# Optimization experiments

Measured on AMD Instinct MI355X. Metric: run time of the kernel, lower is better.

## Reference

```python
import jax, jax.numpy as jnp
import numpy as np

LAYERS = [256, 512, 512, 256]
DIM = 20
BATCH = 131072
PERIOD = 0.1
AMP = 1.0


def tri(x):
    # triangle wave centered around 0 with period PERIOD, amplitude AMP
    # matches: amplitude/period * (period - abs(x % (2p) - p) - p/2)
    return AMP / PERIOD * (PERIOD - jnp.abs(jnp.mod(x, 2.0 * PERIOD) - PERIOD) - PERIOD / 2.0)


def cdist(a, b):
    # pairwise euclidean distance between rows of a [m,d] and b [n,d] -> [m,n]
    d2 = (jnp.sum(a * a, axis=1)[:, None]
          + jnp.sum(b * b, axis=1)[None, :]
          - 2.0 * (a @ b.T))
    return jnp.sqrt(jnp.maximum(d2, 0.0))


def setup_inputs() -> dict:
    key = jax.random.key(0)
    ks = jax.random.split(key, 1 + len(LAYERS) + len(LAYERS))
    inp = {"x": jax.random.normal(ks[0], (BATCH, LAYERS[0]), dtype=jnp.float32)}
    # layer_params: uniform in [-1, 1), shape [l, DIM]
    for i, l in enumerate(LAYERS):
        inp[f"p{i}"] = jax.random.uniform(ks[1 + i], (l, DIM), dtype=jnp.float32,
                                          minval=-1.0, maxval=1.0)
    # layer_biases: uniform in [-0.1, 0.1), shape [l, 1]; only indices 1..n-1 are used
    for i in (1, 2, 3):
        inp[f"b{i}"] = jax.random.uniform(ks[1 + len(LAYERS) + i], (LAYERS[i], 1),
                                          dtype=jnp.float32, minval=-1.0, maxval=1.0) * 0.1
    return inp


def reference(x, p0, p1, p2, p3, b1, b2, b3):
    params = [p0, p1, p2, p3]
    biases = [None, b1, b2, b3]
    n = len(params)
    z = x
    for i in range(n - 1):
        l, lnext = params[i], params[i + 1]
        # synthesized weight: [l_i, l_{i+1}]
        W = tri(cdist(l, lnext)) / np.sqrt(l.shape[0]).astype(np.float32)
        z = z @ W + biases[i + 1].T  # bias [l_{i+1},1].T broadcasts over batch
        if i < n - 2:
            z = jax.nn.relu(z)
    return z
```

## Files before the change

### kernel.cpp

```cpp
#include <hip/hip_runtime.h>
#include <hip/hip_fp16.h>

typedef _Float16 f16x8 __attribute__((ext_vector_type(8)));
typedef _Float16 f16x4 __attribute__((ext_vector_type(4)));
typedef float    f32x4 __attribute__((ext_vector_type(4)));

#define BATCH 131072

__global__ void synth_weights_kernel(const float* __restrict__ p0, const float* __restrict__ p1,
                                     const float* __restrict__ p2, const float* __restrict__ p3,
                                     _Float16* __restrict__ wt0, _Float16* __restrict__ wt1,
                                     _Float16* __restrict__ wt2)
{
    int idx = blockIdx.x * blockDim.x + threadIdx.x;
    const float* A; const float* B; _Float16* Wt; float scl; int e, k, n;
    if (idx < 131072)      { A = p0; B = p1; Wt = wt0; scl = 0.0625f;              e = idx;          k = e & 255; n = e >> 8; }
    else if (idx < 393216) { A = p1; B = p2; Wt = wt1; scl = 0.04419417382415922f; e = idx - 131072; k = e & 511; n = e >> 9; }
    else                   { A = p2; B = p3; Wt = wt2; scl = 0.04419417382415922f; e = idx - 393216; k = e & 511; n = e >> 9; }
    float d2 = 0.f;
#pragma unroll
    for (int t = 0; t < 20; ++t) {
        float df = A[k * 20 + t] - B[n * 20 + t];
        d2 += df * df;
    }
    float d  = sqrtf(d2);
    float md = fmodf(d, 0.2f);
    float w  = 10.0f * (0.05f - fabsf(md - 0.1f)) * scl;
    Wt[(size_t)e] = (_Float16)w;
}

__device__ __forceinline__ f16x8 ld_act(const char* act, int mi, int rl, int hi, int w)
{
    const int row = mi * 16 + rl;
    const int c   = w * 4 + hi;
    return *(const f16x8*)(act + row * 1024 + ((c ^ (row & 7)) << 4));
}

template<int K, int NI, int MI>
__device__ __forceinline__ void mm_reg(const char* act, const _Float16* __restrict__ Wt,
                                       int wc, int lane, int wid, f32x4 (&acc)[NI][MI])
{
    constexpr int NW = K / 32;
    const int rl = lane & 15;
    const int hi = lane >> 4;
    const int ph = (wid * (NW / 8)) & (NW - 1);

    const _Float16* wp[NI];
#pragma unroll
    for (int ni = 0; ni < NI; ++ni)
        wp[ni] = Wt + (size_t)(wc + ni * 16 + rl) * K + hi * 8;

    f16x8 wfA[NI], wfB[NI];
#pragma unroll
    for (int ni = 0; ni < NI; ++ni) wfA[ni] = *(const f16x8*)(wp[ni] + ph * 32);

#pragma unroll 1
    for (int w0 = 0; w0 < NW; w0 += 2) {
        const int wA = (w0 + ph) & (NW - 1);
        const int wB = (w0 + 1 + ph) & (NW - 1);
#pragma unroll
        for (int ni = 0; ni < NI; ++ni) wfB[ni] = *(const f16x8*)(wp[ni] + wB * 32);
        {
            f16x8 xf[MI];
#pragma unroll
            for (int mi = 0; mi < MI; ++mi) xf[mi] = ld_act(act, mi, rl, hi, wA);
            __builtin_amdgcn_s_setprio(1);
#pragma unroll
            for (int ni = 0; ni < NI; ++ni)
#pragma unroll
                for (int mi = 0; mi < MI; ++mi)
                    acc[ni][mi] = __builtin_amdgcn_mfma_f32_16x16x32_f16(wfA[ni], xf[mi], acc[ni][mi], 0, 0, 0);
            __builtin_amdgcn_s_setprio(0);
        }
        if (w0 + 2 < NW) {
            const int wC = (w0 + 2 + ph) & (NW - 1);
#pragma unroll
            for (int ni = 0; ni < NI; ++ni) wfA[ni] = *(const f16x8*)(wp[ni] + wC * 32);
        }
        {
            f16x8 xf[MI];
#pragma unroll
            for (int mi = 0; mi < MI; ++mi) xf[mi] = ld_act(act, mi, rl, hi, wB);
            __builtin_amdgcn_s_setprio(1);
#pragma unroll
            for (int ni = 0; ni < NI; ++ni)
#pragma unroll
                for (int mi = 0; mi < MI; ++mi)
                    acc[ni][mi] = __builtin_amdgcn_mfma_f32_16x16x32_f16(wfB[ni], xf[mi], acc[ni][mi], 0, 0, 0);
            __builtin_amdgcn_s_setprio(0);
        }
    }
}

template<int NI, int MI>
__device__ __forceinline__ void store_z(char* act, const float* __restrict__ bias,
                                        int wc, int lane, f32x4 (&acc)[NI][MI])
{
    const int rl = lane & 15;
    const int hi = lane >> 4;
#pragma unroll
    for (int ni = 0; ni < NI; ++ni) {
        const int n0 = wc + ni * 16 + hi * 4;
        const float4 bv = *(const float4*)(bias + n0);
#pragma unroll
        for (int mi = 0; mi < MI; ++mi) {
            const int m = mi * 16 + rl;
            f16x4 h;
            h[0] = (_Float16)fmaxf(acc[ni][mi][0] + bv.x, 0.0f);
            h[1] = (_Float16)fmaxf(acc[ni][mi][1] + bv.y, 0.0f);
            h[2] = (_Float16)fmaxf(acc[ni][mi][2] + bv.z, 0.0f);
            h[3] = (_Float16)fmaxf(acc[ni][mi][3] + bv.w, 0.0f);
            *(f16x4*)(act + m * 1024 + (((n0 >> 3) ^ (m & 7)) << 4) + (n0 & 7) * 2) = h;
        }
    }
}

__global__ __launch_bounds__(512, 2)
void fused_mlp_kernel(const float* __restrict__ x,
                      const _Float16* __restrict__ wt0, const _Float16* __restrict__ wt1,
                      const _Float16* __restrict__ wt2,
                      const float* __restrict__ b1, const float* __restrict__ b2,
                      const float* __restrict__ b3,
                      float* __restrict__ out)
{
    extern __shared__ char act[];
    const int tid  = threadIdx.x;
    const int lane = tid & 63;
    const int wid  = tid >> 6;
    const size_t m0 = (size_t)blockIdx.x * 128;

#pragma unroll
    for (int it = 0; it < 8; ++it) {
        const int c   = it * 512 + tid;
        const int row = c >> 5;
        const int c8  = c & 31;
        const float* src = x + (m0 + row) * 256 + c8 * 8;
        const float4 v0 = *(const float4*)src;
        const float4 v1 = *(const float4*)(src + 4);
        f16x8 h;
        h[0] = (_Float16)v0.x; h[1] = (_Float16)v0.y; h[2] = (_Float16)v0.z; h[3] = (_Float16)v0.w;
        h[4] = (_Float16)v1.x; h[5] = (_Float16)v1.y; h[6] = (_Float16)v1.z; h[7] = (_Float16)v1.w;
        *(f16x8*)(act + row * 1024 + ((c8 ^ (row & 7)) << 4)) = h;
    }
    __syncthreads();

    const int wc = wid * 64;

    {
        f32x4 acc[4][8] = {};
        mm_reg<256, 4, 8>(act, wt0, wc, lane, wid, acc);
        __syncthreads();
        store_z<4, 8>(act, b1, wc, lane, acc);
        __syncthreads();
    }

    {
        f32x4 acc[4][8] = {};
        mm_reg<512, 4, 8>(act, wt1, wc, lane, wid, acc);
        __syncthreads();
        store_z<4, 8>(act, b2, wc, lane, acc);
        __syncthreads();
    }

    {
        const int wc3 = wid * 32;
        f32x4 acc[2][8] = {};
        mm_reg<512, 2, 8>(act, wt2, wc3, lane, wid, acc);

        const int rl = lane & 15;
        const int hi = lane >> 4;
#pragma unroll
        for (int ni = 0; ni < 2; ++ni) {
            const int n0 = wc3 + ni * 16 + hi * 4;
            const float4 bv = *(const float4*)(b3 + n0);
#pragma unroll
            for (int mi = 0; mi < 8; ++mi) {
                const size_t m = m0 + mi * 16 + rl;
                f32x4 o;
                o[0] = acc[ni][mi][0] + bv.x;
                o[1] = acc[ni][mi][1] + bv.y;
                o[2] = acc[ni][mi][2] + bv.z;
                o[3] = acc[ni][mi][3] + bv.w;
                *(f32x4*)(out + m * 256 + n0) = o;
            }
        }
    }
}

extern "C" void kernel_launch(void* const* d_in, const int* in_sizes, int n_in,
                              void* d_out, int out_size, void* d_ws, size_t ws_size,
                              hipStream_t stream)
{
    const float* x  = (const float*)d_in[0];
    const float* p0 = (const float*)d_in[1];
    const float* p1 = (const float*)d_in[2];
    const float* p2 = (const float*)d_in[3];
    const float* p3 = (const float*)d_in[4];
    const float* b1 = (const float*)d_in[5];
    const float* b2 = (const float*)d_in[6];
    const float* b3 = (const float*)d_in[7];

    char* ws = (char*)d_ws;
    _Float16* wt0 = (_Float16*)(ws);
    _Float16* wt1 = (_Float16*)(ws + 262144);
    _Float16* wt2 = (_Float16*)(ws + 262144 + 524288);

    synth_weights_kernel<<<2048, 256, 0, stream>>>(p0, p1, p2, p3, wt0, wt1, wt2);

    fused_mlp_kernel<<<BATCH / 128, 512, 131072, stream>>>(x, wt0, wt1, wt2, b1, b2, b3,
                                                           (float*)d_out);
}
```

Measured before the change: 186.8 us.

## Pre-swizzle synthesized weights into per-lane fragment-order blobs for coalesced loads

The weight synthesis kernel now writes each weight matrix in the exact order the MFMA fragments are consumed: per wave, per k-step, per n-tile, with each lane's 8 halves contiguous. The MLP kernel then loads a fragment with a single contiguous 1 KB access per wave instead of strided row reads across K. This is meant to cut the number of global/L2 transactions for weight streaming. The MFMA loop order is also swapped to iterate ni inside mi.

```diff
diff --git a/kernel.cpp b/kernel.cpp
--- a/kernel.cpp
+++ b/kernel.cpp
@@ -9,14 +9,30 @@
 
 __global__ void synth_weights_kernel(const float* __restrict__ p0, const float* __restrict__ p1,
                                      const float* __restrict__ p2, const float* __restrict__ p3,
-                                     _Float16* __restrict__ wt0, _Float16* __restrict__ wt1,
-                                     _Float16* __restrict__ wt2)
-{
-    int idx = blockIdx.x * blockDim.x + threadIdx.x;
-    const float* A; const float* B; _Float16* Wt; float scl; int e, k, n;
-    if (idx < 131072)      { A = p0; B = p1; Wt = wt0; scl = 0.0625f;              e = idx;          k = e & 255; n = e >> 8; }
-    else if (idx < 393216) { A = p1; B = p2; Wt = wt1; scl = 0.04419417382415922f; e = idx - 131072; k = e & 511; n = e >> 9; }
-    else                   { A = p2; B = p3; Wt = wt2; scl = 0.04419417382415922f; e = idx - 393216; k = e & 511; n = e >> 9; }
+                                     _Float16* __restrict__ blob0, _Float16* __restrict__ blob1,
+                                     _Float16* __restrict__ blob2)
+{
+    const int idx = blockIdx.x * blockDim.x + threadIdx.x;
+    const float* A; const float* B; _Float16* Wt; float scl; int e, n, k;
+    if (idx < 131072) {
+        A = p0; B = p1; Wt = blob0; scl = 0.0625f; e = idx;
+        const int j = e & 7, lane = (e >> 3) & 63, t = e >> 9;
+        const int ni = t & 3, pw = t >> 2, w = pw & 7, wid = pw >> 3;
+        n = wid * 64 + ni * 16 + (lane & 15);
+        k = w * 32 + ((lane >> 4) << 3) + j;
+    } else if (idx < 393216) {
+        A = p1; B = p2; Wt = blob1; scl = 0.04419417382415922f; e = idx - 131072;
+        const int j = e & 7, lane = (e >> 3) & 63, t = e >> 9;
+        const int ni = t & 3, pw = t >> 2, w = pw & 15, wid = pw >> 4;
+        n = wid * 64 + ni * 16 + (lane & 15);
+        k = w * 32 + ((lane >> 4) << 3) + j;
+    } else {
+        A = p2; B = p3; Wt = blob2; scl = 0.04419417382415922f; e = idx - 393216;
+        const int j = e & 7, lane = (e >> 3) & 63, t = e >> 9;
+        const int ni = t & 1, pw = t >> 1, w = pw & 15, wid = pw >> 4;
+        n = wid * 32 + ni * 16 + (lane & 15);
+        k = w * 32 + ((lane >> 4) << 3) + j;
+    }
     float d2 = 0.f;
 #pragma unroll
     for (int t = 0; t < 20; ++t) {
@@ -36,46 +52,45 @@
     return *(const f16x8*)(act + row * 1024 + ((c ^ (row & 7)) << 4));
 }
 
-template<int K, int NI, int MI>
-__device__ __forceinline__ void mm_reg(const char* act, const _Float16* __restrict__ Wt,
-                                       int wc, int lane, int wid, f32x4 (&acc)[NI][MI])
-{
-    constexpr int NW = K / 32;
+template<int NW, int NI, int MI>
+__device__ __forceinline__ void mm_reg(const char* act, const _Float16* __restrict__ blob,
+                                       int lane, int wid, f32x4 (&acc)[NI][MI])
+{
     const int rl = lane & 15;
     const int hi = lane >> 4;
     const int ph = (wid * (NW / 8)) & (NW - 1);
 
-    const _Float16* wp[NI];
+    const char* wbase = (const char*)blob + ((size_t)wid * NW * NI) * 1024 + lane * 16;
+
+    f16x8 wfA[NI], wfB[NI];
 #pragma unroll
     for (int ni = 0; ni < NI; ++ni)
-        wp[ni] = Wt + (size_t)(wc + ni * 16 + rl) * K + hi * 8;
-
-    f16x8 wfA[NI], wfB[NI];
-#pragma unroll
-    for (int ni = 0; ni < NI; ++ni) wfA[ni] = *(const f16x8*)(wp[ni] + ph * 32);
+        wfA[ni] = *(const f16x8*)(wbase + (ph * NI + ni) * 1024);
 
 #pragma unroll 1
     for (int w0 = 0; w0 < NW; w0 += 2) {
         const int wA = (w0 + ph) & (NW - 1);
         const int wB = (w0 + 1 + ph) & (NW - 1);
 #pragma unroll
-        for (int ni = 0; ni < NI; ++ni) wfB[ni] = *(const f16x8*)(wp[ni] + wB * 32);
+        for (int ni = 0; ni < NI; ++ni)
+            wfB[ni] = *(const f16x8*)(wbase + (wB * NI + ni) * 1024);
         {
             f16x8 xf[MI];
 #pragma unroll
             for (int mi = 0; mi < MI; ++mi) xf[mi] = ld_act(act, mi, rl, hi, wA);
             __builtin_amdgcn_s_setprio(1);
 #pragma unroll
-            for (int ni = 0; ni < NI; ++ni)
-#pragma unroll
-                for (int mi = 0; mi < MI; ++mi)
+            for (int mi = 0; mi < MI; ++mi)
+#pragma unroll
+                for (int ni = 0; ni < NI; ++ni)
                     acc[ni][mi] = __builtin_amdgcn_mfma_f32_16x16x32_f16(wfA[ni], xf[mi], acc[ni][mi], 0, 0, 0);
             __builtin_amdgcn_s_setprio(0);
         }
         if (w0 + 2 < NW) {
             const int wC = (w0 + 2 + ph) & (NW - 1);
 #pragma unroll
-            for (int ni = 0; ni < NI; ++ni) wfA[ni] = *(const f16x8*)(wp[ni] + wC * 32);
+            for (int ni = 0; ni < NI; ++ni)
+                wfA[ni] = *(const f16x8*)(wbase + (wC * NI + ni) * 1024);
         }
         {
             f16x8 xf[MI];
@@ -83,9 +98,9 @@
             for (int mi = 0; mi < MI; ++mi) xf[mi] = ld_act(act, mi, rl, hi, wB);
             __builtin_amdgcn_s_setprio(1);
 #pragma unroll
-            for (int ni = 0; ni < NI; ++ni)
-#pragma unroll
-                for (int mi = 0; mi < MI; ++mi)
+            for (int mi = 0; mi < MI; ++mi)
+#pragma unroll
+                for (int ni = 0; ni < NI; ++ni)
                     acc[ni][mi] = __builtin_amdgcn_mfma_f32_16x16x32_f16(wfB[ni], xf[mi], acc[ni][mi], 0, 0, 0);
             __builtin_amdgcn_s_setprio(0);
         }
@@ -117,8 +132,8 @@
 
 __global__ __launch_bounds__(512, 2)
 void fused_mlp_kernel(const float* __restrict__ x,
-                      const _Float16* __restrict__ wt0, const _Float16* __restrict__ wt1,
-                      const _Float16* __restrict__ wt2,
+                      const _Float16* __restrict__ blob0, const _Float16* __restrict__ blob1,
+                      const _Float16* __restrict__ blob2,
                       const float* __restrict__ b1, const float* __restrict__ b2,
                       const float* __restrict__ b3,
                       float* __restrict__ out)
@@ -148,7 +163,7 @@
 
     {
         f32x4 acc[4][8] = {};
-        mm_reg<256, 4, 8>(act, wt0, wc, lane, wid, acc);
+        mm_reg<8, 4, 8>(act, blob0, lane, wid, acc);
         __syncthreads();
         store_z<4, 8>(act, b1, wc, lane, acc);
         __syncthreads();
@@ -156,7 +171,7 @@
 
     {
         f32x4 acc[4][8] = {};
-        mm_reg<512, 4, 8>(act, wt1, wc, lane, wid, acc);
+        mm_reg<16, 4, 8>(act, blob1, lane, wid, acc);
         __syncthreads();
         store_z<4, 8>(act, b2, wc, lane, acc);
         __syncthreads();
@@ -165,7 +180,7 @@
     {
         const int wc3 = wid * 32;
         f32x4 acc[2][8] = {};
-        mm_reg<512, 2, 8>(act, wt2, wc3, lane, wid, acc);
+        mm_reg<16, 2, 8>(act, blob2, lane, wid, acc);
 
         const int rl = lane & 15;
         const int hi = lane >> 4;
@@ -201,12 +216,12 @@
     const float* b3 = (const float*)d_in[7];
 
     char* ws = (char*)d_ws;
-    _Float16* wt0 = (_Float16*)(ws);
-    _Float16* wt1 = (_Float16*)(ws + 262144);
-    _Float16* wt2 = (_Float16*)(ws + 262144 + 524288);
-
-    synth_weights_kernel<<<2048, 256, 0, stream>>>(p0, p1, p2, p3, wt0, wt1, wt2);
-
-    fused_mlp_kernel<<<BATCH / 128, 512, 131072, stream>>>(x, wt0, wt1, wt2, b1, b2, b3,
-                                                           (float*)d_out);
-}
+    _Float16* blob0 = (_Float16*)(ws);
+    _Float16* blob1 = (_Float16*)(ws + 262144);
+    _Float16* blob2 = (_Float16*)(ws + 262144 + 524288);
+
+    synth_weights_kernel<<<2048, 256, 0, stream>>>(p0, p1, p2, p3, blob0, blob1, blob2);
+
+    fused_mlp_kernel<<<BATCH / 128, 512, 131072, stream>>>(x, blob0, blob1, blob2,
+                                                           b1, b2, b3, (float*)d_out);
+}
```

Result: faster. 159.9 us (-14.4%).
